# Kernel optimization log

Hardware: AMD Instinct MI355X
Metric: run time of the kernel (lower is better)

## Reference

```python
import jax, jax.numpy as jnp
import numpy as np

B, S, D, H = 2, 2048, 2048, 16
HD = D // H
F = 4 * D
EPS = 1e-8


def _layernorm(x, g, b):
    m = jnp.mean(x, axis=-1, keepdims=True)
    v = jnp.mean((x - m) ** 2, axis=-1, keepdims=True)
    return (x - m) / jnp.sqrt(v + EPS) * g + b


def setup_inputs() -> dict:
    key = jax.random.key(0)
    ks = jax.random.split(key, 12)

    def lin(k, fan_in, fan_out):
        # torch Linear init ~ U(-1/sqrt(fan_in), 1/sqrt(fan_in)); stored as [in, out]
        lim = 1.0 / np.sqrt(fan_in)
        kw, kb = jax.random.split(k)
        w = jax.random.uniform(kw, (fan_in, fan_out), jnp.float32, -lim, lim)
        b = jax.random.uniform(kb, (fan_out,), jnp.float32, -lim, lim)
        return w, b

    x = jax.random.normal(ks[0], (B, S, D), jnp.float32)
    wq, bq = lin(ks[1], D, D)
    wk, bk = lin(ks[2], D, D)
    wv, bv = lin(ks[3], D, D)
    wo, bo = lin(ks[4], D, D)
    wu, bu = lin(ks[5], D, F)
    wd, bd = lin(ks[6], F, D)
    g1 = jnp.ones((D,), jnp.float32)
    b1 = jnp.zeros((D,), jnp.float32)
    g2 = jnp.ones((D,), jnp.float32)
    b2 = jnp.zeros((D,), jnp.float32)
    return dict(x=x, wq=wq, bq=bq, wk=wk, bk=bk, wv=wv, bv=bv, wo=wo, bo=bo,
                g1=g1, b1=b1, wu=wu, bu=bu, wd=wd, bd=bd, g2=g2, b2=b2)


def reference(x, wq, bq, wk, bk, wv, bv, wo, bo, g1, b1, wu, bu, wd, bd, g2, b2):
    b, s, d = x.shape
    # QKV projections -> [b, H, s, HD]
    q = (x @ wq + bq).reshape(b, s, H, HD).transpose(0, 2, 1, 3)
    k = (x @ wk + bk).reshape(b, s, H, HD).transpose(0, 2, 1, 3)
    v = (x @ wv + bv).reshape(b, s, H, HD).transpose(0, 2, 1, 3)
    # scaled dot-product with causal mask filled at -1e9 (matches masked_fill)
    scores = jnp.einsum('bhqd,bhkd->bhqk', q, k) / np.sqrt(HD).astype(np.float32)
    causal = jnp.tril(jnp.ones((s, s), bool))
    scores = jnp.where(causal, scores, jnp.float32(-1e9))
    attn = jax.nn.softmax(scores, axis=-1)  # dropout is identity (eval / rate=0)
    o = jnp.einsum('bhqk,bhkd->bhqd', attn, v)
    o = o.transpose(0, 2, 1, 3).reshape(b, s, d)
    o = o @ wo + bo
    x = _layernorm(x + o, g1, b1)
    # FFN with exact (erf) GELU, residual, LN
    h = jax.nn.gelu(x @ wu + bu, approximate=False)
    h = h @ wd + bd
    return _layernorm(x + h, g2, b2)
```

## Files before the change

kernel.cpp:

```cpp
#include <hip/hip_runtime.h>
#include <hip/hip_bf16.h>
#include <math.h>

#define DEV __device__ __forceinline__

typedef __bf16 bf16x8 __attribute__((ext_vector_type(8)));
typedef float f32x4 __attribute__((ext_vector_type(4)));
typedef unsigned short ushort_t;
typedef ushort_t us8 __attribute__((ext_vector_type(8)));
typedef ushort_t us4 __attribute__((ext_vector_type(4)));

DEV float bf2f(ushort_t u) {
    unsigned v = ((unsigned)u) << 16;
    float f; __builtin_memcpy(&f, &v, 4); return f;
}
DEV ushort_t f2bf(float f) {
    unsigned u; __builtin_memcpy(&u, &f, 4);
    u += 0x7fffu + ((u >> 16) & 1);
    return (ushort_t)(u >> 16);
}

DEV void gload16(const void* g, void* l) {
    __builtin_amdgcn_global_load_lds(
        (const __attribute__((address_space(1))) void*)g,
        (__attribute__((address_space(3))) void*)l, 16, 0, 0);
}

__global__ __launch_bounds__(256) void fill_kernel(float* out, long n, float v) {
    long i = (long)blockIdx.x * blockDim.x + threadIdx.x;
    if (i < n) out[i] = v;
}

__global__ __launch_bounds__(256) void cast_bf16_kernel(
    const float* __restrict__ in, ushort_t* __restrict__ out, long n)
{
    long i = ((long)blockIdx.x * blockDim.x + threadIdx.x) * 4;
    if (i >= n) return;
    float4 v = *(const float4*)(in + i);
    us4 o = { f2bf(v.x), f2bf(v.y), f2bf(v.z), f2bf(v.w) };
    *(us4*)(out + i) = o;
}

__global__ __launch_bounds__(256) void transpose_bf16_kernel(
    const float* __restrict__ in, ushort_t* __restrict__ out, int R, int C)
{
    __shared__ float tile[32][33];
    int c0 = blockIdx.x * 32, r0 = blockIdx.y * 32;
    int tx = threadIdx.x & 31, ty = threadIdx.x >> 5;
#pragma unroll
    for (int j = 0; j < 4; ++j) {
        int r = ty + j * 8;
        tile[r][tx] = in[(long)(r0 + r) * C + (c0 + tx)];
    }
    __syncthreads();
#pragma unroll
    for (int j = 0; j < 4; ++j) {
        int r = ty + j * 8;
        out[(long)(c0 + r) * R + (r0 + tx)] = f2bf(tile[tx][r]);
    }
}

__global__ __launch_bounds__(256) void gemm_bt_kernel(
    const ushort_t* __restrict__ A, const ushort_t* __restrict__ Bt,
    const float* __restrict__ bias, ushort_t* __restrict__ C,
    int M, int N, int K, int act)
{
    __shared__ __align__(16) ushort_t lA[128 * 64];
    __shared__ __align__(16) ushort_t lB[128 * 64];
    const int t = threadIdx.x;
    const int w = t >> 6, l = t & 63;
    const int wr = w >> 1, wc = w & 1;
    const long m0 = (long)blockIdx.x * 128;
    const long n0 = (long)blockIdx.y * 128;

    const int sr = l >> 3;
    const int scol = (l & 7) * 16;

    f32x4 acc[4][4];
    f32x4 zf = {0.f, 0.f, 0.f, 0.f};
#pragma unroll
    for (int i = 0; i < 4; ++i)
#pragma unroll
        for (int j = 0; j < 4; ++j) acc[i][j] = zf;

    const char* Ab = (const char*)(A + m0 * K);
    const char* Bb = (const char*)(Bt + n0 * K);
    char* lAc = (char*)lA;
    char* lBc = (char*)lB;

    for (int k0 = 0; k0 < K; k0 += 64) {
        __syncthreads();
#pragma unroll
        for (int c = 0; c < 4; ++c) {
            int row = (w * 4 + c) * 8 + sr;
            int src = scol ^ ((row & 7) << 4);
            gload16(Ab + (long)row * (K * 2) + (long)k0 * 2 + src, lAc + (w * 4 + c) * 1024);
            gload16(Bb + (long)row * (K * 2) + (long)k0 * 2 + src, lBc + (w * 4 + c) * 1024);
        }
        __syncthreads();
#pragma unroll
        for (int ks = 0; ks < 2; ++ks) {
            bf16x8 af[4], bfr[4];
#pragma unroll
            for (int i = 0; i < 4; ++i) {
                int row = wr * 64 + i * 16 + (l & 15);
                int cb = (ks * 64 + (l >> 4) * 16) ^ ((row & 7) << 4);
                af[i] = *(const bf16x8*)(lAc + row * 128 + cb);
            }
#pragma unroll
            for (int j = 0; j < 4; ++j) {
                int row = wc * 64 + j * 16 + (l & 15);
                int cb = (ks * 64 + (l >> 4) * 16) ^ ((row & 7) << 4);
                bfr[j] = *(const bf16x8*)(lBc + row * 128 + cb);
            }
#pragma unroll
            for (int i = 0; i < 4; ++i)
#pragma unroll
                for (int j = 0; j < 4; ++j)
                    acc[i][j] = __builtin_amdgcn_mfma_f32_16x16x32_bf16(af[i], bfr[j], acc[i][j], 0, 0, 0);
        }
    }

#pragma unroll
    for (int j = 0; j < 4; ++j) {
        int col = (int)n0 + wc * 64 + j * 16 + (l & 15);
        float bv = bias[col];
#pragma unroll
        for (int i = 0; i < 4; ++i) {
            long rowb = m0 + wr * 64 + i * 16 + (l >> 4) * 4;
#pragma unroll
            for (int r = 0; r < 4; ++r) {
                float v2 = acc[i][j][r] + bv;
                if (act == 1) v2 = 0.5f * v2 * (1.f + erff(v2 * 0.70710678118654752440f));
                C[(rowb + r) * (long)N + col] = f2bf(v2);
            }
        }
    }
}

__global__ __launch_bounds__(256) void attn_kernel(
    const ushort_t* __restrict__ qkv, ushort_t* __restrict__ o)
{
    __shared__ __align__(16) ushort_t lK[32 * 128];
    __shared__ __align__(16) ushort_t lV[128 * 48];
    __shared__ __align__(16) ushort_t lP[4 * 16 * 32];

    const int t = threadIdx.x, w = t >> 6, l = t & 63;
    const int qblk = blockIdx.x, bh = blockIdx.y;
    const int b = bh >> 4, h = bh & 15;
    const int q0 = qblk * 64 + w * 16;
    const long base = (long)b * 2048 * 6144 + (long)h * 128;

    const ushort_t* qrow = qkv + base + (long)(q0 + (l & 15)) * 6144;
    bf16x8 qf[4];
#pragma unroll
    for (int hb = 0; hb < 4; ++hb)
        qf[hb] = *(const bf16x8*)(qrow + hb * 32 + (l >> 4) * 8);

    f32x4 accO[8];
    f32x4 zf = {0.f, 0.f, 0.f, 0.f};
#pragma unroll
    for (int i = 0; i < 8; ++i) accO[i] = zf;
    float m_r[4] = {-1e30f, -1e30f, -1e30f, -1e30f};
    float l_r[4] = {0.f, 0.f, 0.f, 0.f};

    const int nkv = qblk * 64 + 64;
    const float scale = 0.08838834764831845f;
    const char* lKc = (const char*)lK;

    for (int kv0 = 0; kv0 < nkv; kv0 += 32) {
        __syncthreads();
#pragma unroll
        for (int c = 0; c < 2; ++c) {
            int chunk = w * 2 + c;
            int row = chunk * 4 + (l >> 4);
            int src = ((l & 15) * 16) ^ ((row & 7) << 4);
            const char* gK = (const char*)(qkv + base + 2048 + (long)(kv0 + row) * 6144) + src;
            gload16(gK, (char*)lK + chunk * 1024);
        }
        {
            int kvi = t & 31;
            int hd0 = (t >> 5) * 8;
#pragma unroll
            for (int half = 0; half < 2; ++half) {
                int hdb = hd0 + half * 64;
                us8 vv = *(const us8*)(qkv + base + 4096 + (long)(kv0 + kvi) * 6144 + hdb);
#pragma unroll
                for (int j = 0; j < 8; ++j)
                    lV[(hdb + j) * 48 + kvi] = vv[j];
            }
        }
        __syncthreads();

        if (kv0 <= q0 + 15) {
            f32x4 sc[2];
#pragma unroll
            for (int kvs = 0; kvs < 2; ++kvs) {
                sc[kvs] = zf;
                int row = kvs * 16 + (l & 15);
#pragma unroll
                for (int hb = 0; hb < 4; ++hb) {
                    int cb = (hb * 64 + (l >> 4) * 16) ^ ((row & 7) << 4);
                    bf16x8 kf = *(const bf16x8*)(lKc + row * 256 + cb);
                    sc[kvs] = __builtin_amdgcn_mfma_f32_16x16x32_bf16(qf[hb], kf, sc[kvs], 0, 0, 0);
                }
            }
#pragma unroll
            for (int r = 0; r < 4; ++r) {
                int qg = q0 + (l >> 4) * 4 + r;
                float s0 = sc[0][r] * scale;
                float s1 = sc[1][r] * scale;
                if (kv0 + (l & 15) > qg) s0 = -1e30f;
                if (kv0 + 16 + (l & 15) > qg) s1 = -1e30f;
                float pm = fmaxf(s0, s1);
                pm = fmaxf(pm, __shfl_xor(pm, 1));
                pm = fmaxf(pm, __shfl_xor(pm, 2));
                pm = fmaxf(pm, __shfl_xor(pm, 4));
                pm = fmaxf(pm, __shfl_xor(pm, 8));
                float mn = fmaxf(m_r[r], pm);
                float p0 = __expf(s0 - mn);
                float p1 = __expf(s1 - mn);
                float ps = p0 + p1;
                ps += __shfl_xor(ps, 1);
                ps += __shfl_xor(ps, 2);
                ps += __shfl_xor(ps, 4);
                ps += __shfl_xor(ps, 8);
                float alpha = __expf(m_r[r] - mn);
                l_r[r] = l_r[r] * alpha + ps;
                m_r[r] = mn;
#pragma unroll
                for (int tt = 0; tt < 8; ++tt) accO[tt][r] *= alpha;
                int qloc = (l >> 4) * 4 + r;
                lP[w * 512 + qloc * 32 + (l & 15)] = f2bf(p0);
                lP[w * 512 + qloc * 32 + 16 + (l & 15)] = f2bf(p1);
            }
            asm volatile("s_waitcnt lgkmcnt(0)" ::: "memory");
            bf16x8 pf = *(const bf16x8*)(lP + w * 512 + (l & 15) * 32 + (l >> 4) * 8);
#pragma unroll
            for (int tt = 0; tt < 8; ++tt) {
                int hd = tt * 16 + (l & 15);
                bf16x8 vf = *(const bf16x8*)(lV + hd * 48 + (l >> 4) * 8);
                accO[tt] = __builtin_amdgcn_mfma_f32_16x16x32_bf16(pf, vf, accO[tt], 0, 0, 0);
            }
        }
    }

    const long obase = (long)b * 2048 * 2048 + (long)h * 128;
#pragma unroll
    for (int r = 0; r < 4; ++r) {
        float inv = 1.f / l_r[r];
        long orow = obase + (long)(q0 + (l >> 4) * 4 + r) * 2048;
#pragma unroll
        for (int tt = 0; tt < 8; ++tt)
            o[orow + tt * 16 + (l & 15)] = f2bf(accO[tt][r] * inv);
    }
}

__global__ __launch_bounds__(256) void ln_kernel(
    const float* xres, const ushort_t* __restrict__ addb,
    const float* __restrict__ g, const float* __restrict__ bb,
    float* outf, ushort_t* __restrict__ outb)
{
    __shared__ float rs[4], rss[4];
    const int row = blockIdx.x, t = threadIdx.x;
    const float* xp = xres + (long)row * 2048 + t * 8;
    const ushort_t* ap = addb + (long)row * 2048 + t * 8;
    float4 a = *(const float4*)xp;
    float4 c = *(const float4*)(xp + 4);
    us8 ad = *(const us8*)ap;
    float v[8];
    v[0] = a.x + bf2f(ad[0]); v[1] = a.y + bf2f(ad[1]);
    v[2] = a.z + bf2f(ad[2]); v[3] = a.w + bf2f(ad[3]);
    v[4] = c.x + bf2f(ad[4]); v[5] = c.y + bf2f(ad[5]);
    v[6] = c.z + bf2f(ad[6]); v[7] = c.w + bf2f(ad[7]);
    float s = 0.f, ss = 0.f;
#pragma unroll
    for (int j = 0; j < 8; ++j) { s += v[j]; ss += v[j] * v[j]; }
#pragma unroll
    for (int off = 32; off > 0; off >>= 1) {
        s += __shfl_down(s, off);
        ss += __shfl_down(ss, off);
    }
    if ((t & 63) == 0) { rs[t >> 6] = s; rss[t >> 6] = ss; }
    __syncthreads();
    float S = rs[0] + rs[1] + rs[2] + rs[3];
    float SS = rss[0] + rss[1] + rss[2] + rss[3];
    float mean = S * (1.f / 2048.f);
    float var = SS * (1.f / 2048.f) - mean * mean;
    float rstd = rsqrtf(var + 1e-8f);
    float of[8];
#pragma unroll
    for (int j = 0; j < 8; ++j) {
        int col = t * 8 + j;
        of[j] = (v[j] - mean) * rstd * g[col] + bb[col];
    }
    float4 o1 = {of[0], of[1], of[2], of[3]};
    float4 o2 = {of[4], of[5], of[6], of[7]};
    float* op = outf + (long)row * 2048 + t * 8;
    *(float4*)op = o1;
    *(float4*)(op + 4) = o2;
    if (outb) {
        us8 ob;
#pragma unroll
        for (int j = 0; j < 8; ++j) ob[j] = f2bf(of[j]);
        *(us8*)(outb + (long)row * 2048 + t * 8) = ob;
    }
}

extern "C" void kernel_launch(void* const* d_in, const int* in_sizes, int n_in,
                              void* d_out, int out_size, void* d_ws, size_t ws_size,
                              hipStream_t stream)
{
    const float* x  = (const float*)d_in[0];
    const float* wq = (const float*)d_in[1];
    const float* bq = (const float*)d_in[2];
    const float* wk = (const float*)d_in[3];
    const float* bk = (const float*)d_in[4];
    const float* wv = (const float*)d_in[5];
    const float* bv = (const float*)d_in[6];
    const float* wo = (const float*)d_in[7];
    const float* bo = (const float*)d_in[8];
    const float* g1 = (const float*)d_in[9];
    const float* b1 = (const float*)d_in[10];
    const float* wu = (const float*)d_in[11];
    const float* bu = (const float*)d_in[12];
    const float* wd = (const float*)d_in[13];
    const float* bd = (const float*)d_in[14];
    const float* g2 = (const float*)d_in[15];
    const float* b2 = (const float*)d_in[16];
    (void)in_sizes; (void)n_in; (void)out_size;

    const size_t MB = 1ull << 20;
    char* wsp = (char*)d_ws;
    char*  slotA = wsp;
    char*  slotB = wsp + 32 * MB;
    char*  slotC = wsp + 48 * MB;
    float* bqkv  = (float*)(wsp + 112 * MB);
    const size_t need = 112 * MB + 32768;
    if (ws_size < need) {
        fill_kernel<<<(8388608 + 255) / 256, 256, 0, stream>>>((float*)d_out, 8388608L, 1e6f);
        return;
    }

    ushort_t* xb   = (ushort_t*)slotB;
    ushort_t* wT   = (ushort_t*)slotA;
    ushort_t* qkvb = (ushort_t*)slotC;
    ushort_t* ab   = (ushort_t*)slotB;
    ushort_t* pb   = (ushort_t*)slotC;
    float*    x1f  = (float*)d_out;
    ushort_t* x1b  = (ushort_t*)slotB;
    ushort_t* hb   = (ushort_t*)slotC;
    ushort_t* db   = (ushort_t*)slotB;

    cast_bf16_kernel<<<8192, 256, 0, stream>>>(x, xb, 8388608L);
    transpose_bf16_kernel<<<dim3(64, 64), 256, 0, stream>>>(wq, wT, 2048, 2048);
    transpose_bf16_kernel<<<dim3(64, 64), 256, 0, stream>>>(wk, wT + 2048ull * 2048, 2048, 2048);
    transpose_bf16_kernel<<<dim3(64, 64), 256, 0, stream>>>(wv, wT + 2ull * 2048 * 2048, 2048, 2048);
    hipMemcpyAsync(bqkv,        bq, 2048 * sizeof(float), hipMemcpyDeviceToDevice, stream);
    hipMemcpyAsync(bqkv + 2048, bk, 2048 * sizeof(float), hipMemcpyDeviceToDevice, stream);
    hipMemcpyAsync(bqkv + 4096, bv, 2048 * sizeof(float), hipMemcpyDeviceToDevice, stream);
    gemm_bt_kernel<<<dim3(32, 48), 256, 0, stream>>>(xb, wT, bqkv, qkvb, 4096, 6144, 2048, 0);
    attn_kernel<<<dim3(32, 32), 256, 0, stream>>>(qkvb, ab);
    transpose_bf16_kernel<<<dim3(64, 64), 256, 0, stream>>>(wo, wT, 2048, 2048);
    gemm_bt_kernel<<<dim3(32, 16), 256, 0, stream>>>(ab, wT, bo, pb, 4096, 2048, 2048, 0);
    ln_kernel<<<4096, 256, 0, stream>>>(x, pb, g1, b1, x1f, x1b);
    transpose_bf16_kernel<<<dim3(256, 64), 256, 0, stream>>>(wu, wT, 2048, 8192);
    gemm_bt_kernel<<<dim3(32, 64), 256, 0, stream>>>(x1b, wT, bu, hb, 4096, 8192, 2048, 1);
    transpose_bf16_kernel<<<dim3(64, 256), 256, 0, stream>>>(wd, wT, 8192, 2048);
    gemm_bt_kernel<<<dim3(32, 16), 256, 0, stream>>>(hb, wT, bd, db, 4096, 2048, 8192, 0);
    ln_kernel<<<4096, 256, 0, stream>>>(x1f, db, g2, b2, (float*)d_out, nullptr);
}
```

Measured before the change: 835.0 us.

## Double-buffer K/V tiles and enlarge attention blocks to 128 queries and 64 keys

Restructures the causal attention kernel to use 8-wave blocks covering 128 query rows and 64-key tiles instead of 32. The next K tile is prefetched into a second LDS buffer via global_load_lds, and the next V tile is prefetched into registers while the current tile is computed. V is transposed into LDS with packed 32-bit writes. The aim is to hide global load latency, halve the number of barrier-separated iterations and raise MFMA work per sync, at the cost of more LDS and register use and fewer, larger blocks.

```diff
diff --git a/kernel.cpp b/kernel.cpp
--- a/kernel.cpp
+++ b/kernel.cpp
@@ -138,18 +138,21 @@
     }
 }
 
-__global__ __launch_bounds__(256) void attn_kernel(
+__global__ __launch_bounds__(512, 4) void attn_kernel(
     const ushort_t* __restrict__ qkv, ushort_t* __restrict__ o)
 {
-    __shared__ __align__(16) ushort_t lK[32 * 128];
-    __shared__ __align__(16) ushort_t lV[128 * 48];
-    __shared__ __align__(16) ushort_t lP[4 * 16 * 32];
+    __shared__ __align__(16) ushort_t lK[2 * 64 * 128];
+    __shared__ __align__(16) ushort_t lVT[128 * 72];
+    __shared__ __align__(16) ushort_t lP[8 * 16 * 64];
 
     const int t = threadIdx.x, w = t >> 6, l = t & 63;
     const int qblk = blockIdx.x, bh = blockIdx.y;
     const int b = bh >> 4, h = bh & 15;
-    const int q0 = qblk * 64 + w * 16;
+    const int q0 = qblk * 128 + w * 16;
     const long base = (long)b * 2048 * 6144 + (long)h * 128;
+    const ushort_t* Kg = qkv + base + 2048;
+    const ushort_t* Vg = qkv + base + 4096;
+    char* lKc = (char*)lK;
 
     const ushort_t* qrow = qkv + base + (long)(q0 + (l & 15)) * 6144;
     bf16x8 qf[4];
@@ -164,63 +167,79 @@
     float m_r[4] = {-1e30f, -1e30f, -1e30f, -1e30f};
     float l_r[4] = {0.f, 0.f, 0.f, 0.f};
 
-    const int nkv = qblk * 64 + 64;
+    const int nt = (qblk * 128 + 128) >> 6;
     const float scale = 0.08838834764831845f;
-    const char* lKc = (const char*)lK;
-
-    for (int kv0 = 0; kv0 < nkv; kv0 += 32) {
-        __syncthreads();
-#pragma unroll
-        for (int c = 0; c < 2; ++c) {
-            int chunk = w * 2 + c;
-            int row = chunk * 4 + (l >> 4);
+
+    const int kvp = t & 31;
+    const int d0 = (t >> 5) * 8;
+    us8 va, vb;
+
+    auto stageK = [&](int kt, int buf) {
+#pragma unroll
+        for (int i = 0; i < 2; ++i) {
+            int c = w * 2 + i;
+            int row = c * 4 + (l >> 4);
             int src = ((l & 15) * 16) ^ ((row & 7) << 4);
-            const char* gK = (const char*)(qkv + base + 2048 + (long)(kv0 + row) * 6144) + src;
-            gload16(gK, (char*)lK + chunk * 1024);
-        }
-        {
-            int kvi = t & 31;
-            int hd0 = (t >> 5) * 8;
-#pragma unroll
-            for (int half = 0; half < 2; ++half) {
-                int hdb = hd0 + half * 64;
-                us8 vv = *(const us8*)(qkv + base + 4096 + (long)(kv0 + kvi) * 6144 + hdb);
-#pragma unroll
-                for (int j = 0; j < 8; ++j)
-                    lV[(hdb + j) * 48 + kvi] = vv[j];
-            }
-        }
-        __syncthreads();
-
+            gload16((const char*)(Kg + (long)(kt * 64 + row) * 6144) + src,
+                    lKc + buf * 16384 + c * 1024);
+        }
+    };
+    auto loadV = [&](int kt) {
+        const ushort_t* vr = Vg + (long)(kt * 64 + kvp * 2) * 6144 + d0;
+        va = *(const us8*)vr;
+        vb = *(const us8*)(vr + 6144);
+    };
+    auto writeVT = [&]() {
+#pragma unroll
+        for (int j = 0; j < 8; ++j) {
+            unsigned pk = (unsigned)va[j] | ((unsigned)vb[j] << 16);
+            *(unsigned*)(lVT + (d0 + j) * 72 + kvp * 2) = pk;
+        }
+    };
+
+    stageK(0, 0);
+    loadV(0);
+    asm volatile("s_waitcnt vmcnt(0)" ::: "memory");
+    writeVT();
+    __syncthreads();
+
+    for (int t0 = 0; t0 < nt; ++t0) {
+        const int cur = t0 & 1;
+        const bool more = (t0 + 1 < nt);
+        if (more) { stageK(t0 + 1, cur ^ 1); loadV(t0 + 1); }
+
+        const int kv0 = t0 * 64;
         if (kv0 <= q0 + 15) {
-            f32x4 sc[2];
-#pragma unroll
-            for (int kvs = 0; kvs < 2; ++kvs) {
+            f32x4 sc[4];
+#pragma unroll
+            for (int kvs = 0; kvs < 4; ++kvs) {
                 sc[kvs] = zf;
                 int row = kvs * 16 + (l & 15);
 #pragma unroll
                 for (int hb = 0; hb < 4; ++hb) {
                     int cb = (hb * 64 + (l >> 4) * 16) ^ ((row & 7) << 4);
-                    bf16x8 kf = *(const bf16x8*)(lKc + row * 256 + cb);
+                    bf16x8 kf = *(const bf16x8*)(lKc + cur * 16384 + row * 256 + cb);
                     sc[kvs] = __builtin_amdgcn_mfma_f32_16x16x32_bf16(qf[hb], kf, sc[kvs], 0, 0, 0);
                 }
             }
 #pragma unroll
             for (int r = 0; r < 4; ++r) {
                 int qg = q0 + (l >> 4) * 4 + r;
-                float s0 = sc[0][r] * scale;
-                float s1 = sc[1][r] * scale;
-                if (kv0 + (l & 15) > qg) s0 = -1e30f;
-                if (kv0 + 16 + (l & 15) > qg) s1 = -1e30f;
-                float pm = fmaxf(s0, s1);
+                float s[4];
+#pragma unroll
+                for (int kvs = 0; kvs < 4; ++kvs) {
+                    s[kvs] = sc[kvs][r] * scale;
+                    if (kv0 + kvs * 16 + (l & 15) > qg) s[kvs] = -1e30f;
+                }
+                float pm = fmaxf(fmaxf(s[0], s[1]), fmaxf(s[2], s[3]));
                 pm = fmaxf(pm, __shfl_xor(pm, 1));
                 pm = fmaxf(pm, __shfl_xor(pm, 2));
                 pm = fmaxf(pm, __shfl_xor(pm, 4));
                 pm = fmaxf(pm, __shfl_xor(pm, 8));
                 float mn = fmaxf(m_r[r], pm);
-                float p0 = __expf(s0 - mn);
-                float p1 = __expf(s1 - mn);
-                float ps = p0 + p1;
+                float p[4], ps = 0.f;
+#pragma unroll
+                for (int kvs = 0; kvs < 4; ++kvs) { p[kvs] = __expf(s[kvs] - mn); ps += p[kvs]; }
                 ps += __shfl_xor(ps, 1);
                 ps += __shfl_xor(ps, 2);
                 ps += __shfl_xor(ps, 4);
@@ -231,18 +250,25 @@
 #pragma unroll
                 for (int tt = 0; tt < 8; ++tt) accO[tt][r] *= alpha;
                 int qloc = (l >> 4) * 4 + r;
-                lP[w * 512 + qloc * 32 + (l & 15)] = f2bf(p0);
-                lP[w * 512 + qloc * 32 + 16 + (l & 15)] = f2bf(p1);
+#pragma unroll
+                for (int kvs = 0; kvs < 4; ++kvs)
+                    lP[w * 1024 + qloc * 64 + kvs * 16 + (l & 15)] = f2bf(p[kvs]);
             }
             asm volatile("s_waitcnt lgkmcnt(0)" ::: "memory");
-            bf16x8 pf = *(const bf16x8*)(lP + w * 512 + (l & 15) * 32 + (l >> 4) * 8);
-#pragma unroll
-            for (int tt = 0; tt < 8; ++tt) {
-                int hd = tt * 16 + (l & 15);
-                bf16x8 vf = *(const bf16x8*)(lV + hd * 48 + (l >> 4) * 8);
-                accO[tt] = __builtin_amdgcn_mfma_f32_16x16x32_bf16(pf, vf, accO[tt], 0, 0, 0);
-            }
-        }
+#pragma unroll
+            for (int ks = 0; ks < 2; ++ks) {
+                bf16x8 pf = *(const bf16x8*)(lP + w * 1024 + (l & 15) * 64 + ks * 32 + (l >> 4) * 8);
+#pragma unroll
+                for (int tt = 0; tt < 8; ++tt) {
+                    bf16x8 vf = *(const bf16x8*)(lVT + (tt * 16 + (l & 15)) * 72 + ks * 32 + (l >> 4) * 8);
+                    accO[tt] = __builtin_amdgcn_mfma_f32_16x16x32_bf16(pf, vf, accO[tt], 0, 0, 0);
+                }
+            }
+        }
+
+        asm volatile("s_waitcnt vmcnt(0)" ::: "memory");
+        __syncthreads();
+        if (more) { writeVT(); __syncthreads(); }
     }
 
     const long obase = (long)b * 2048 * 2048 + (long)h * 128;
@@ -360,7 +386,7 @@
     hipMemcpyAsync(bqkv + 2048, bk, 2048 * sizeof(float), hipMemcpyDeviceToDevice, stream);
     hipMemcpyAsync(bqkv + 4096, bv, 2048 * sizeof(float), hipMemcpyDeviceToDevice, stream);
     gemm_bt_kernel<<<dim3(32, 48), 256, 0, stream>>>(xb, wT, bqkv, qkvb, 4096, 6144, 2048, 0);
-    attn_kernel<<<dim3(32, 32), 256, 0, stream>>>(qkvb, ab);
+    attn_kernel<<<dim3(16, 32), 512, 0, stream>>>(qkvb, ab);
     transpose_bf16_kernel<<<dim3(64, 64), 256, 0, stream>>>(wo, wT, 2048, 2048);
     gemm_bt_kernel<<<dim3(32, 16), 256, 0, stream>>>(ab, wT, bo, pb, 4096, 2048, 2048, 0);
     ln_kernel<<<4096, 256, 0, stream>>>(x, pb, g1, b1, x1f, x1b);
```

Measured after the change: 736.5 us. 11.8% less time.
